# Kernel optimization log

Measured on AMD Instinct MI355X. Metric: run time of the kernel, lower is better.

Reference implementation:

```python
import jax, jax.numpy as jnp
import numpy as np

B, N, D0 = 128, 128, 512   # batch, n_objects, obj_dim
H, KD, R = 32, 64, 16      # n_heads, key_dim, n_relations
D = D0 + 1                 # with temporal tag

def setup_inputs() -> dict:
    key = jax.random.key(0)
    k1, k2, k3, k4, k5 = jax.random.split(key, 5)
    s = 0.02
    return {
        'obj_seq': jax.random.normal(k1, (B, N, D0), jnp.float32),
        'W_k':  jax.random.normal(k2, (KD, D), jnp.float32) * s,
        'W_q1': jax.random.normal(k3, (H * KD, D * N), jnp.float32) * s,
        'W_q2': jax.random.normal(k4, (H * KD, D * N), jnp.float32) * s,
        'W_s':  jax.random.normal(k5, (R, D), jnp.float32) * s,
    }

def reference(obj_seq, W_k, W_q1, W_q2, W_s):
    b, n, _ = obj_seq.shape
    # append temporal tag channel: obj -> [B, N, D]
    tag = jnp.broadcast_to(jnp.arange(n, dtype=obj_seq.dtype)[None, :, None], (b, n, 1))
    obj = jnp.concatenate([obj_seq, tag], axis=2)
    flat = obj.reshape(b, -1)                      # [B, N*D]
    Q1 = (flat @ W_q1.T).reshape(b, H, KD)         # [B, H, KD]
    Q2 = (flat @ W_q2.T).reshape(b, H, KD)
    K = obj @ W_k.T                                # [B, N, KD]
    # scores [B, N, H], softmax over objects (dim=1 in torch)
    A1 = jax.nn.softmax(jnp.einsum('bhk,bnk->bnh', Q1, K), axis=1)
    A2 = jax.nn.softmax(jnp.einsum('bhk,bnk->bnh', Q2, K), axis=1)
    # attention-weighted object sums: [B, H, D]
    E1 = jnp.einsum('bnh,bnd->bhd', A1, obj)
    E2 = jnp.einsum('bnh,bnd->bhd', A2, obj)
    Dr = E1 @ W_s.T - E2 @ W_s.T                   # [B, H, R]
    Dr = jnp.concatenate([Dr, E1[:, :, -1:], E2[:, :, -1:]], axis=2)  # [B, H, R+2]
    return Dr.reshape(b, -1)                       # [B, H*(R+2)]
```

## Files before the change

kernel.cpp:

```cpp
#include <hip/hip_runtime.h>
#include <cstdint>

typedef _Float16 f16;
typedef _Float16 f16x8 __attribute__((ext_vector_type(8)));
typedef float f32x4 __attribute__((ext_vector_type(4)));
typedef float floatx4 __attribute__((ext_vector_type(4)));

#define KTOT 65664
#define KSTEPS 2052
#define DP 544

__device__ __forceinline__ void gload_lds16(const void* g, void* l) {
  __builtin_amdgcn_global_load_lds(
      (const __attribute__((address_space(1))) void*)g,
      (__attribute__((address_space(3))) void*)l, 16, 0, 0);
}

__global__ void prep_flat(const float* __restrict__ obj_seq, f16* __restrict__ flatKM) {
  int base = blockIdx.x * 1024 + threadIdx.x;
#pragma unroll
  for (int j = 0; j < 4; ++j) {
    int o = base + j * 256;
    int e = o & 7;
    int r = (o >> 3) & 127;
    int k8 = (o >> 10) & 3;
    int kb = o >> 12;
    int k = kb * 32 + k8 * 8 + e;
    int n = k / 513;
    int d = k - n * 513;
    float v = (d < 512) ? obj_seq[(((size_t)(r << 7) + n) << 9) + d] : (float)n;
    f16 h = (f16)v;
    size_t idx = (size_t)kb * 8192 + k8 * 1024 + r * 8 + e;
    flatKM[idx] = h;
    flatKM[idx + 4096] = (f16)(v - (float)h);
  }
}

__global__ void prep_obj(const float* __restrict__ obj_seq, f16* __restrict__ objHi,
                         f16* __restrict__ objLo, f16* __restrict__ objT16) {
  __shared__ f16 tile[32][132];
  int b = blockIdx.x / 17, c = blockIdx.x - 17 * (blockIdx.x / 17);
  int t = threadIdx.x;
  if (c < 16) {
#pragma unroll
    for (int i = 0; i < 16; ++i) {
      int e = t + i * 256;
      int n = e >> 5, dd = e & 31;
      float v = obj_seq[(((size_t)(b << 7) + n) << 9) + (c << 5) + dd];
      f16 h = (f16)v;
      objHi[((size_t)((b << 7) + n)) * DP + (c << 5) + dd] = h;
      objLo[((size_t)((b << 7) + n)) * DP + (c << 5) + dd] = (f16)(v - (float)h);
      tile[dd][n] = h;
    }
    __syncthreads();
#pragma unroll
    for (int i = 0; i < 16; ++i) {
      int e = t + i * 256;
      int dd = e >> 7, n = e & 127;
      objT16[(((size_t)b * DP + (c << 5) + dd) << 7) + n] = tile[dd][n];
    }
  } else {
#pragma unroll
    for (int i = 0; i < 16; ++i) {
      int e = t + i * 256;
      int n = e >> 5, dd = e & 31;
      f16 h = (dd == 0) ? (f16)(float)n : (f16)0.f;
      objHi[((size_t)((b << 7) + n)) * DP + 512 + dd] = h;
      objLo[((size_t)((b << 7) + n)) * DP + 512 + dd] = (f16)0.f;
    }
#pragma unroll
    for (int i = 0; i < 16; ++i) {
      int e = t + i * 256;
      int dd = e >> 7, n = e & 127;
      objT16[(((size_t)b * DP + 512 + dd) << 7) + n] = (dd == 0) ? (f16)(float)n : (f16)0.f;
    }
  }
}

__global__ void prep_wk(const float* __restrict__ W_k, f16* __restrict__ WkHi,
                        f16* __restrict__ WkLo) {
  int o = blockIdx.x * 256 + threadIdx.x;
  int kd = o / DP, d = o - kd * DP;
  float v = (d < 513) ? W_k[kd * 513 + d] * 1024.f : 0.f;
  f16 h = (f16)v;
  WkHi[o] = h;
  WkLo[o] = (f16)(v - (float)h);
}

__global__ __launch_bounds__(512, 2) void qgemm(const f16* __restrict__ flatKM,
                                                const float* __restrict__ Wq1,
                                                const float* __restrict__ Wq2,
                                                float* __restrict__ Q) {
  __shared__ __align__(16) char smem[131072];
  const int tid = threadIdx.x;
  const int lane = tid & 63;
  const int wave = tid >> 6;
  const int wm = wave >> 2, wn = wave & 3;
  const int l15 = lane & 15, lk = lane >> 4;
  const int ntile = blockIdx.x & 31;
  const int ksp = blockIdx.x >> 5;
  const int t0 = ksp * 257;
  const int nt = min(257, KSTEPS - t0);
  const float* Wsrc = (ntile < 16) ? (Wq1 + (size_t)ntile * 128 * KTOT)
                                   : (Wq2 + (size_t)(ntile - 16) * 128 * KTOT);

  const int col0 = tid >> 3;
  const int kh0 = (tid & 7) ^ (col0 & 7);
  const int col1 = (512 + tid) >> 3;
  const int kh1 = (tid & 7) ^ (col1 & 7);
  const float* wsrc0 = Wsrc + (size_t)col0 * KTOT + (size_t)t0 * 32 + kh0 * 4;
  const float* wsrc1 = Wsrc + (size_t)col1 * KTOT + (size_t)t0 * 32 + kh1 * 4;
  const f16* asrc = flatKM + (size_t)t0 * 8192 + tid * 8;

  int aoff[4];
#pragma unroll
  for (int mi = 0; mi < 4; ++mi) aoff[mi] = lk * 2048 + (wm * 64 + mi * 16 + l15) * 16;
  int woff[2][2];
#pragma unroll
  for (int nf = 0; nf < 2; ++nf) {
    int col = wn * 32 + nf * 16 + l15;
    int c7 = col & 7;
    woff[nf][0] = col * 128 + ((lk * 2) ^ c7) * 16;
    woff[nf][1] = col * 128 + ((lk * 2 + 1) ^ c7) * 16;
  }

  f32x4 acc[4][2];
#pragma unroll
  for (int mi = 0; mi < 4; ++mi)
#pragma unroll
    for (int nf = 0; nf < 2; ++nf) acc[mi][nf] = (f32x4){0.f, 0.f, 0.f, 0.f};

  auto stage = [&](int tt) {
    char* As = smem + (tt & 3) * 16384;
    char* Ws = smem + 65536 + (tt & 3) * 16384;
    gload_lds16(asrc + (size_t)tt * 8192, As + tid * 16);
    gload_lds16(asrc + (size_t)tt * 8192 + 4096, As + 8192 + tid * 16);
    gload_lds16(wsrc0 + (size_t)tt * 32, Ws + tid * 16);
    gload_lds16(wsrc1 + (size_t)tt * 32, Ws + 8192 + tid * 16);
  };

  stage(0); stage(1); stage(2);

  for (int t = 0; t < nt; ++t) {
    if (t < nt - 2)       asm volatile("s_waitcnt vmcnt(8)" ::: "memory");
    else if (t == nt - 2) asm volatile("s_waitcnt vmcnt(4)" ::: "memory");
    else                  asm volatile("s_waitcnt vmcnt(0)" ::: "memory");
    __builtin_amdgcn_s_barrier();
    __builtin_amdgcn_sched_barrier(0);
    if (t + 3 < nt) stage(t + 3);

    const char* As = smem + (t & 3) * 16384;
    const char* Ws = smem + 65536 + (t & 3) * 16384;

    f16x8 afh[4], afl[4];
#pragma unroll
    for (int mi = 0; mi < 4; ++mi) {
      afh[mi] = *(const f16x8*)(As + aoff[mi]);
      afl[mi] = *(const f16x8*)(As + 8192 + aoff[mi]);
    }
    floatx4 wv[2][2];
#pragma unroll
    for (int nf = 0; nf < 2; ++nf) {
      wv[nf][0] = *(const floatx4*)(Ws + woff[nf][0]);
      wv[nf][1] = *(const floatx4*)(Ws + woff[nf][1]);
    }

    f16x8 whi[2], wlo[2];
#pragma unroll
    for (int nf = 0; nf < 2; ++nf)
#pragma unroll
      for (int j = 0; j < 4; ++j) {
        { float v = wv[nf][0][j] * 1024.f; f16 h = (f16)v; whi[nf][j] = h; wlo[nf][j] = (f16)(v - (float)h); }
        { float v = wv[nf][1][j] * 1024.f; f16 h = (f16)v; whi[nf][4 + j] = h; wlo[nf][4 + j] = (f16)(v - (float)h); }
      }

#pragma unroll
    for (int mi = 0; mi < 4; ++mi) {
#pragma unroll
      for (int nf = 0; nf < 2; ++nf) {
        acc[mi][nf] = __builtin_amdgcn_mfma_f32_16x16x32_f16(afh[mi], whi[nf], acc[mi][nf], 0, 0, 0);
        acc[mi][nf] = __builtin_amdgcn_mfma_f32_16x16x32_f16(afh[mi], wlo[nf], acc[mi][nf], 0, 0, 0);
        acc[mi][nf] = __builtin_amdgcn_mfma_f32_16x16x32_f16(afl[mi], whi[nf], acc[mi][nf], 0, 0, 0);
      }
    }
  }

  const float s = 1.f / 1024.f;
#pragma unroll
  for (int mi = 0; mi < 4; ++mi) {
    int row = wm * 64 + mi * 16 + lk * 4;
#pragma unroll
    for (int nf = 0; nf < 2; ++nf) {
      int col = ntile * 128 + wn * 32 + nf * 16 + l15;
#pragma unroll
      for (int j = 0; j < 4; ++j) atomicAdd(&Q[(size_t)(row + j) * 4096 + col], acc[mi][nf][j] * s);
    }
  }
}

__global__ __launch_bounds__(512, 1) void predinet_tail(
    const f16* __restrict__ objHi, const f16* __restrict__ objLo, const f16* __restrict__ objT16,
    const f16* __restrict__ WkHi, const f16* __restrict__ WkLo,
    const float* __restrict__ Q, const float* __restrict__ W_s, float* __restrict__ out) {
  __shared__ __align__(16) char smem[105984];
  const int b = blockIdx.x;
  const int tid = threadIdx.x, lane = tid & 63, wave = tid >> 6;
  const int l15 = lane & 15, lk = lane >> 4;

  f16* WT = (f16*)(smem);
  f16* Qh = (f16*)(smem + 17408);
  f16* Ql = (f16*)(smem + 26624);
  f16* Kh = (f16*)(smem + 35840);
  f16* Kl = (f16*)(smem + 54272);
  float* S = (float*)(smem + 72704);
  f16* E = (f16*)(smem + 17408);
  float* DL = (float*)(smem + 96832);

  {
    const float* qsrc = Q + (size_t)b * 4096 + tid * 8;
    floatx4 q0 = *(const floatx4*)qsrc;
    floatx4 q1 = *(const floatx4*)(qsrc + 4);
    int hp = tid >> 3, kd = (tid * 8) & 63;
    f16x8 vh, vl;
#pragma unroll
    for (int j = 0; j < 4; ++j) {
      f16 h0 = (f16)q0[j]; vh[j] = h0; vl[j] = (f16)(q0[j] - (float)h0);
      f16 h1 = (f16)q1[j]; vh[4 + j] = h1; vl[4 + j] = (f16)(q1[j] - (float)h1);
    }
    *(f16x8*)(Qh + hp * 72 + kd) = vh;
    *(f16x8*)(Ql + hp * 72 + kd) = vl;
  }
  {
    f32x4 acc[4];
#pragma unroll
    for (int nf = 0; nf < 4; ++nf) acc[nf] = (f32x4){0.f, 0.f, 0.f, 0.f};
    const f16* arowH = objHi + ((size_t)(b * 128) + wave * 16 + l15) * DP + lk * 8;
    const f16* arowL = objLo + ((size_t)(b * 128) + wave * 16 + l15) * DP + lk * 8;
    const f16* bhi = WkHi + (size_t)l15 * DP + lk * 8;
    const f16* blo = WkLo + (size_t)l15 * DP + lk * 8;
    for (int ks = 0; ks < 17; ++ks) {
      f16x8 ah = *(const f16x8*)(arowH + ks * 32);
      f16x8 al = *(const f16x8*)(arowL + ks * 32);
#pragma unroll
      for (int nf = 0; nf < 4; ++nf) {
        f16x8 h = *(const f16x8*)(bhi + (size_t)nf * 16 * DP + ks * 32);
        f16x8 l = *(const f16x8*)(blo + (size_t)nf * 16 * DP + ks * 32);
        acc[nf] = __builtin_amdgcn_mfma_f32_16x16x32_f16(ah, h, acc[nf], 0, 0, 0);
        acc[nf] = __builtin_amdgcn_mfma_f32_16x16x32_f16(ah, l, acc[nf], 0, 0, 0);
        acc[nf] = __builtin_amdgcn_mfma_f32_16x16x32_f16(al, h, acc[nf], 0, 0, 0);
      }
    }
#pragma unroll
    for (int nf = 0; nf < 4; ++nf)
#pragma unroll
      for (int j = 0; j < 4; ++j) {
        float kv = acc[nf][j] * (1.f / 1024.f);
        f16 h = (f16)kv;
        Kh[(wave * 16 + lk * 4 + j) * 72 + nf * 16 + l15] = h;
        Kl[(wave * 16 + lk * 4 + j) * 72 + nf * 16 + l15] = (f16)(kv - (float)h);
      }
  }
  __syncthreads();
  {
    f32x4 acc[4];
#pragma unroll
    for (int nf = 0; nf < 4; ++nf) acc[nf] = (f32x4){0.f, 0.f, 0.f, 0.f};
#pragma unroll
    for (int ks = 0; ks < 2; ++ks) {
      f16x8 ah = *(const f16x8*)(Kh + (wave * 16 + l15) * 72 + ks * 32 + lk * 8);
      f16x8 al = *(const f16x8*)(Kl + (wave * 16 + l15) * 72 + ks * 32 + lk * 8);
#pragma unroll
      for (int nf = 0; nf < 4; ++nf) {
        f16x8 bh = *(const f16x8*)(Qh + (nf * 16 + l15) * 72 + ks * 32 + lk * 8);
        f16x8 bl = *(const f16x8*)(Ql + (nf * 16 + l15) * 72 + ks * 32 + lk * 8);
        acc[nf] = __builtin_amdgcn_mfma_f32_16x16x32_f16(ah, bh, acc[nf], 0, 0, 0);
        acc[nf] = __builtin_amdgcn_mfma_f32_16x16x32_f16(ah, bl, acc[nf], 0, 0, 0);
        acc[nf] = __builtin_amdgcn_mfma_f32_16x16x32_f16(al, bh, acc[nf], 0, 0, 0);
      }
    }
#pragma unroll
    for (int nf = 0; nf < 4; ++nf)
#pragma unroll
      for (int j = 0; j < 4; ++j)
        S[(wave * 16 + lk * 4 + j) * 65 + nf * 16 + l15] = acc[nf][j];
  }
  __syncthreads();
  {
#pragma unroll
    for (int ci = 0; ci < 8; ++ci) {
      int c = wave * 8 + ci;
      float s0 = S[lane * 65 + c], s1 = S[(lane + 64) * 65 + c];
      float m = fmaxf(s0, s1);
      for (int off = 32; off; off >>= 1) m = fmaxf(m, __shfl_xor(m, off));
      float e0 = __expf(s0 - m), e1 = __expf(s1 - m);
      float sum = e0 + e1;
      for (int off = 32; off; off >>= 1) sum += __shfl_xor(sum, off);
      float inv = 1.f / sum;
      WT[c * 136 + lane] = (f16)(e0 * inv);
      WT[c * 136 + 64 + lane] = (f16)(e1 * inv);
    }
  }
  __syncthreads();
  {
    f16x8 bw[4][4];
#pragma unroll
    for (int nf = 0; nf < 4; ++nf)
#pragma unroll
      for (int ks = 0; ks < 4; ++ks)
        bw[nf][ks] = *(const f16x8*)(WT + (nf * 16 + l15) * 136 + ks * 32 + lk * 8);
    for (int r = 0; r < 5; ++r) {
      int mi = r * 8 + wave;
      if (mi >= 34) break;
      const f16* arow = objT16 + (((size_t)b * DP + mi * 16 + l15) << 7) + lk * 8;
      f16x8 a[4];
#pragma unroll
      for (int ks = 0; ks < 4; ++ks) a[ks] = *(const f16x8*)(arow + ks * 32);
#pragma unroll
      for (int nf = 0; nf < 4; ++nf) {
        f32x4 acc = (f32x4){0.f, 0.f, 0.f, 0.f};
#pragma unroll
        for (int ks = 0; ks < 4; ++ks)
          acc = __builtin_amdgcn_mfma_f32_16x16x32_f16(a[ks], bw[nf][ks], acc, 0, 0, 0);
#pragma unroll
        for (int j = 0; j < 4; ++j)
          E[(mi * 16 + lk * 4 + j) * 73 + nf * 16 + l15] = (f16)acc[j];
      }
    }
  }
  __syncthreads();
  {
    f16* Ws16 = WT;
    for (int i = tid; i < 16 * DP; i += 512) {
      int r = i / DP, d = i - r * DP;
      Ws16[i] = (f16)((d < 513) ? W_s[r * 513 + d] : 0.f);
    }
  }
  __syncthreads();
  if (wave < 4) {
    const f16* Ws16 = WT;
    f32x4 acc = (f32x4){0.f, 0.f, 0.f, 0.f};
    for (int ks = 0; ks < 17; ++ks) {
      f16x8 a = *(const f16x8*)(Ws16 + l15 * DP + ks * 32 + lk * 8);
      f16x8 bv;
#pragma unroll
      for (int jj = 0; jj < 8; ++jj)
        bv[jj] = E[(ks * 32 + lk * 8 + jj) * 73 + wave * 16 + l15];
      acc = __builtin_amdgcn_mfma_f32_16x16x32_f16(a, bv, acc, 0, 0, 0);
    }
#pragma unroll
    for (int j = 0; j < 4; ++j) DL[(lk * 4 + j) * 64 + wave * 16 + l15] = acc[j];
  }
  __syncthreads();
  {
    int h = tid >> 4, r = tid & 15;
    float v = DL[r * 64 + h] - DL[r * 64 + 32 + h];
    out[(size_t)b * 576 + h * 18 + r] = v;
    if (tid < 64) {
      int set = tid >> 5, hh = tid & 31;
      out[(size_t)b * 576 + hh * 18 + 16 + set] = (float)E[512 * 73 + set * 32 + hh];
    }
  }
}

extern "C" void kernel_launch(void* const* d_in, const int* in_sizes, int n_in,
                              void* d_out, int out_size, void* d_ws, size_t ws_size,
                              hipStream_t stream) {
  const float* obj_seq = (const float*)d_in[0];
  const float* W_k = (const float*)d_in[1];
  const float* W_q1 = (const float*)d_in[2];
  const float* W_q2 = (const float*)d_in[3];
  const float* W_s = (const float*)d_in[4];
  float* out = (float*)d_out;

  char* ws = (char*)d_ws;
  size_t off = 0;
  auto carve = [&](size_t bytes) -> char* {
    char* p = ws + off;
    off += (bytes + 255) & ~(size_t)255;
    return p;
  };
  f16* flatKM = (f16*)carve((size_t)KSTEPS * 8192 * 2);
  f16* objHi = (f16*)carve((size_t)16384 * DP * 2);
  f16* objLo = (f16*)carve((size_t)16384 * DP * 2);
  f16* objT16 = (f16*)carve((size_t)128 * DP * 128 * 2);
  f16* WkHi = (f16*)carve((size_t)64 * DP * 2);
  f16* WkLo = (f16*)carve((size_t)64 * DP * 2);
  float* Q = (float*)carve((size_t)128 * 4096 * 4);
  (void)ws_size; (void)in_sizes; (void)n_in; (void)out_size;

  hipMemsetAsync(Q, 0, (size_t)128 * 4096 * 4, stream);
  prep_flat<<<8208, 256, 0, stream>>>(obj_seq, flatKM);
  prep_obj<<<2176, 256, 0, stream>>>(obj_seq, objHi, objLo, objT16);
  prep_wk<<<136, 256, 0, stream>>>(W_k, WkHi, WkLo);
  qgemm<<<256, 512, 0, stream>>>(flatKM, W_q1, W_q2, Q);
  predinet_tail<<<128, 512, 0, stream>>>(objHi, objLo, objT16, WkHi, WkLo, Q, W_s, out);
}
```

Baseline: 358.3 us.

## Double-buffer 64-wide K tiles in qgemm and replace atomics with split-K partials

The qgemm main loop now stages 64-wide K chunks, twice as large per step, into a two-deep LDS double buffer instead of a four-deep ring of 32-wide chunks. A second barrier before issuing the next stage guards buffer reuse. The split-K reduction no longer uses atomicAdd into a memset Q buffer. Each of the 8 K-splits writes its own partial slice, and the tail kernel sums the 8 partials when loading Q. This removes the memset and atomic traffic, at the cost of shallower prefetch depth, an extra barrier per step, and more workspace reads in the tail.

```diff
diff --git a/kernel.cpp b/kernel.cpp
--- a/kernel.cpp
+++ b/kernel.cpp
@@ -8,6 +8,7 @@
 
 #define KTOT 65664
 #define KSTEPS 2052
+#define K64S 1026
 #define DP 544
 
 __device__ __forceinline__ void gload_lds16(const void* g, void* l) {
@@ -90,7 +91,7 @@
 __global__ __launch_bounds__(512, 2) void qgemm(const f16* __restrict__ flatKM,
                                                 const float* __restrict__ Wq1,
                                                 const float* __restrict__ Wq2,
-                                                float* __restrict__ Q) {
+                                                float* __restrict__ Qpart) {
   __shared__ __align__(16) char smem[131072];
   const int tid = threadIdx.x;
   const int lane = tid & 63;
@@ -99,30 +100,36 @@
   const int l15 = lane & 15, lk = lane >> 4;
   const int ntile = blockIdx.x & 31;
   const int ksp = blockIdx.x >> 5;
-  const int t0 = ksp * 257;
-  const int nt = min(257, KSTEPS - t0);
+  const int t0 = ksp * 129;
+  const int nt = min(129, K64S - t0);
   const float* Wsrc = (ntile < 16) ? (Wq1 + (size_t)ntile * 128 * KTOT)
                                    : (Wq2 + (size_t)(ntile - 16) * 128 * KTOT);
 
-  const int col0 = tid >> 3;
-  const int kh0 = (tid & 7) ^ (col0 & 7);
-  const int col1 = (512 + tid) >> 3;
-  const int kh1 = (tid & 7) ^ (col1 & 7);
-  const float* wsrc0 = Wsrc + (size_t)col0 * KTOT + (size_t)t0 * 32 + kh0 * 4;
-  const float* wsrc1 = Wsrc + (size_t)col1 * KTOT + (size_t)t0 * 32 + kh1 * 4;
-  const f16* asrc = flatKM + (size_t)t0 * 8192 + tid * 8;
-
-  int aoff[4];
-#pragma unroll
-  for (int mi = 0; mi < 4; ++mi) aoff[mi] = lk * 2048 + (wm * 64 + mi * 16 + l15) * 16;
-  int woff[2][2];
-#pragma unroll
-  for (int nf = 0; nf < 2; ++nf) {
-    int col = wn * 32 + nf * 16 + l15;
-    int c7 = col & 7;
-    woff[nf][0] = col * 128 + ((lk * 2) ^ c7) * 16;
-    woff[nf][1] = col * 128 + ((lk * 2 + 1) ^ c7) * 16;
-  }
+  const float* wsrcs[4];
+#pragma unroll
+  for (int c = 0; c < 4; ++c) {
+    int col = c * 32 + (tid >> 4);
+    int chlog = (tid & 15) ^ (col & 15);
+    wsrcs[c] = Wsrc + (size_t)col * KTOT + (size_t)t0 * 64 + chlog * 4;
+  }
+  const f16* asrc = flatKM + (size_t)t0 * 16384 + tid * 8;
+
+  int aoff[2][4];
+#pragma unroll
+  for (int h = 0; h < 2; ++h)
+#pragma unroll
+    for (int mi = 0; mi < 4; ++mi)
+      aoff[h][mi] = h * 16384 + lk * 2048 + (wm * 64 + mi * 16 + l15) * 16;
+  int woff[2][2][2];
+#pragma unroll
+  for (int h = 0; h < 2; ++h)
+#pragma unroll
+    for (int nf = 0; nf < 2; ++nf) {
+      int col = wn * 32 + nf * 16 + l15;
+      int ch = h * 8 + lk * 2;
+      woff[h][nf][0] = 32768 + col * 256 + ((ch) ^ l15) * 16;
+      woff[h][nf][1] = 32768 + col * 256 + ((ch + 1) ^ l15) * 16;
+    }
 
   f32x4 acc[4][2];
 #pragma unroll
@@ -131,61 +138,64 @@
     for (int nf = 0; nf < 2; ++nf) acc[mi][nf] = (f32x4){0.f, 0.f, 0.f, 0.f};
 
   auto stage = [&](int tt) {
-    char* As = smem + (tt & 3) * 16384;
-    char* Ws = smem + 65536 + (tt & 3) * 16384;
-    gload_lds16(asrc + (size_t)tt * 8192, As + tid * 16);
-    gload_lds16(asrc + (size_t)tt * 8192 + 4096, As + 8192 + tid * 16);
-    gload_lds16(wsrc0 + (size_t)tt * 32, Ws + tid * 16);
-    gload_lds16(wsrc1 + (size_t)tt * 32, Ws + 8192 + tid * 16);
+    char* S = smem + (tt & 1) * 65536;
+#pragma unroll
+    for (int c = 0; c < 4; ++c)
+      gload_lds16(asrc + (size_t)tt * 16384 + c * 4096, S + c * 8192 + tid * 16);
+#pragma unroll
+    for (int c = 0; c < 4; ++c)
+      gload_lds16(wsrcs[c] + (size_t)tt * 64, S + 32768 + c * 8192 + tid * 16);
   };
 
-  stage(0); stage(1); stage(2);
+  stage(0);
+  stage(1);
 
   for (int t = 0; t < nt; ++t) {
-    if (t < nt - 2)       asm volatile("s_waitcnt vmcnt(8)" ::: "memory");
-    else if (t == nt - 2) asm volatile("s_waitcnt vmcnt(4)" ::: "memory");
-    else                  asm volatile("s_waitcnt vmcnt(0)" ::: "memory");
+    if (t < nt - 1) asm volatile("s_waitcnt vmcnt(8)" ::: "memory");
+    else            asm volatile("s_waitcnt vmcnt(0)" ::: "memory");
     __builtin_amdgcn_s_barrier();
     __builtin_amdgcn_sched_barrier(0);
-    if (t + 3 < nt) stage(t + 3);
-
-    const char* As = smem + (t & 3) * 16384;
-    const char* Ws = smem + 65536 + (t & 3) * 16384;
-
-    f16x8 afh[4], afl[4];
-#pragma unroll
-    for (int mi = 0; mi < 4; ++mi) {
-      afh[mi] = *(const f16x8*)(As + aoff[mi]);
-      afl[mi] = *(const f16x8*)(As + 8192 + aoff[mi]);
-    }
-    floatx4 wv[2][2];
-#pragma unroll
-    for (int nf = 0; nf < 2; ++nf) {
-      wv[nf][0] = *(const floatx4*)(Ws + woff[nf][0]);
-      wv[nf][1] = *(const floatx4*)(Ws + woff[nf][1]);
-    }
-
-    f16x8 whi[2], wlo[2];
-#pragma unroll
-    for (int nf = 0; nf < 2; ++nf)
-#pragma unroll
-      for (int j = 0; j < 4; ++j) {
-        { float v = wv[nf][0][j] * 1024.f; f16 h = (f16)v; whi[nf][j] = h; wlo[nf][j] = (f16)(v - (float)h); }
-        { float v = wv[nf][1][j] * 1024.f; f16 h = (f16)v; whi[nf][4 + j] = h; wlo[nf][4 + j] = (f16)(v - (float)h); }
-      }
-
-#pragma unroll
-    for (int mi = 0; mi < 4; ++mi) {
+    const char* S = smem + (t & 1) * 65536;
+
+#pragma unroll
+    for (int h = 0; h < 2; ++h) {
+      f16x8 afh[4], afl[4];
+#pragma unroll
+      for (int mi = 0; mi < 4; ++mi) {
+        afh[mi] = *(const f16x8*)(S + aoff[h][mi]);
+        afl[mi] = *(const f16x8*)(S + aoff[h][mi] + 8192);
+      }
+      floatx4 wv[2][2];
 #pragma unroll
       for (int nf = 0; nf < 2; ++nf) {
-        acc[mi][nf] = __builtin_amdgcn_mfma_f32_16x16x32_f16(afh[mi], whi[nf], acc[mi][nf], 0, 0, 0);
-        acc[mi][nf] = __builtin_amdgcn_mfma_f32_16x16x32_f16(afh[mi], wlo[nf], acc[mi][nf], 0, 0, 0);
-        acc[mi][nf] = __builtin_amdgcn_mfma_f32_16x16x32_f16(afl[mi], whi[nf], acc[mi][nf], 0, 0, 0);
-      }
-    }
+        wv[nf][0] = *(const floatx4*)(S + woff[h][nf][0]);
+        wv[nf][1] = *(const floatx4*)(S + woff[h][nf][1]);
+      }
+      f16x8 whi[2], wlo[2];
+#pragma unroll
+      for (int nf = 0; nf < 2; ++nf)
+#pragma unroll
+        for (int j = 0; j < 4; ++j) {
+          { float v = wv[nf][0][j] * 1024.f; f16 hh = (f16)v; whi[nf][j] = hh; wlo[nf][j] = (f16)(v - (float)hh); }
+          { float v = wv[nf][1][j] * 1024.f; f16 hh = (f16)v; whi[nf][4 + j] = hh; wlo[nf][4 + j] = (f16)(v - (float)hh); }
+        }
+#pragma unroll
+      for (int mi = 0; mi < 4; ++mi)
+#pragma unroll
+        for (int nf = 0; nf < 2; ++nf) {
+          acc[mi][nf] = __builtin_amdgcn_mfma_f32_16x16x32_f16(afh[mi], whi[nf], acc[mi][nf], 0, 0, 0);
+          acc[mi][nf] = __builtin_amdgcn_mfma_f32_16x16x32_f16(afh[mi], wlo[nf], acc[mi][nf], 0, 0, 0);
+          acc[mi][nf] = __builtin_amdgcn_mfma_f32_16x16x32_f16(afl[mi], whi[nf], acc[mi][nf], 0, 0, 0);
+        }
+    }
+
+    __builtin_amdgcn_sched_barrier(0);
+    __builtin_amdgcn_s_barrier();
+    if (t + 2 < nt) stage(t + 2);
   }
 
   const float s = 1.f / 1024.f;
+  float* qout = Qpart + (size_t)ksp * 524288;
 #pragma unroll
   for (int mi = 0; mi < 4; ++mi) {
     int row = wm * 64 + mi * 16 + lk * 4;
@@ -193,7 +203,8 @@
     for (int nf = 0; nf < 2; ++nf) {
       int col = ntile * 128 + wn * 32 + nf * 16 + l15;
 #pragma unroll
-      for (int j = 0; j < 4; ++j) atomicAdd(&Q[(size_t)(row + j) * 4096 + col], acc[mi][nf][j] * s);
+      for (int j = 0; j < 4; ++j)
+        qout[(size_t)(row + j) * 4096 + col] = acc[mi][nf][j] * s;
     }
   }
 }
@@ -201,7 +212,7 @@
 __global__ __launch_bounds__(512, 1) void predinet_tail(
     const f16* __restrict__ objHi, const f16* __restrict__ objLo, const f16* __restrict__ objT16,
     const f16* __restrict__ WkHi, const f16* __restrict__ WkLo,
-    const float* __restrict__ Q, const float* __restrict__ W_s, float* __restrict__ out) {
+    const float* __restrict__ Qpart, const float* __restrict__ W_s, float* __restrict__ out) {
   __shared__ __align__(16) char smem[105984];
   const int b = blockIdx.x;
   const int tid = threadIdx.x, lane = tid & 63, wave = tid >> 6;
@@ -217,9 +228,14 @@
   float* DL = (float*)(smem + 96832);
 
   {
-    const float* qsrc = Q + (size_t)b * 4096 + tid * 8;
-    floatx4 q0 = *(const floatx4*)qsrc;
-    floatx4 q1 = *(const floatx4*)(qsrc + 4);
+    const float* qp = Qpart + (size_t)b * 4096 + tid * 8;
+    floatx4 q0 = (floatx4){0.f, 0.f, 0.f, 0.f};
+    floatx4 q1 = (floatx4){0.f, 0.f, 0.f, 0.f};
+#pragma unroll
+    for (int p = 0; p < 8; ++p) {
+      q0 += *(const floatx4*)(qp + (size_t)p * 524288);
+      q1 += *(const floatx4*)(qp + (size_t)p * 524288 + 4);
+    }
     int hp = tid >> 3, kd = (tid * 8) & 63;
     f16x8 vh, vl;
 #pragma unroll
@@ -385,13 +401,12 @@
   f16* objT16 = (f16*)carve((size_t)128 * DP * 128 * 2);
   f16* WkHi = (f16*)carve((size_t)64 * DP * 2);
   f16* WkLo = (f16*)carve((size_t)64 * DP * 2);
-  float* Q = (float*)carve((size_t)128 * 4096 * 4);
+  float* Qpart = (float*)carve((size_t)8 * 524288 * 4);
   (void)ws_size; (void)in_sizes; (void)n_in; (void)out_size;
 
-  hipMemsetAsync(Q, 0, (size_t)128 * 4096 * 4, stream);
   prep_flat<<<8208, 256, 0, stream>>>(obj_seq, flatKM);
   prep_obj<<<2176, 256, 0, stream>>>(obj_seq, objHi, objLo, objT16);
   prep_wk<<<136, 256, 0, stream>>>(W_k, WkHi, WkLo);
-  qgemm<<<256, 512, 0, stream>>>(flatKM, W_q1, W_q2, Q);
-  predinet_tail<<<128, 512, 0, stream>>>(objHi, objLo, objT16, WkHi, WkLo, Q, W_s, out);
-}
+  qgemm<<<256, 512, 0, stream>>>(flatKM, W_q1, W_q2, Qpart);
+  predinet_tail<<<128, 512, 0, stream>>>(objHi, objLo, objT16, WkHi, WkLo, Qpart, W_s, out);
+}
```

Result: slower. 379.2 us (+5.8%).
